# Performance work log

Hardware: AMD Instinct MI355X
Metric: run time of the kernel (lower is better)

The kernel has to match this reference:

```python
import jax, jax.numpy as jnp
import numpy as np

B, S, E, D = 8, 2048, 1024, 64


def setup_inputs() -> dict:
    key = jax.random.key(0)
    ks = jax.random.split(key, 8)
    x = jax.random.normal(ks[0], (B, S, E), dtype=jnp.float32)
    mask = jax.random.randint(ks[1], (B, S), 0, 2, dtype=jnp.int32)
    # torch.nn.Linear(E, D): weight [D, E], bias [D]; y = x @ W.T + b
    scale = 0.02
    Wq = jax.random.normal(ks[2], (D, E), dtype=jnp.float32) * scale
    bq = jax.random.normal(ks[3], (D,), dtype=jnp.float32) * scale
    Wk = jax.random.normal(ks[4], (D, E), dtype=jnp.float32) * scale
    bk = jax.random.normal(ks[5], (D,), dtype=jnp.float32) * scale
    Wv = jax.random.normal(ks[6], (D, E), dtype=jnp.float32) * scale
    bv = jax.random.normal(ks[7], (D,), dtype=jnp.float32) * scale
    return {"x": x, "mask": mask, "Wq": Wq, "bq": bq, "Wk": Wk, "bk": bk, "Wv": Wv, "bv": bv}


def reference(x, mask, Wq, bq, Wk, bk, Wv, bv):
    # Linear projections: [B,S,E] @ [E,D] -> [B,S,D]
    q = jnp.einsum('bse,de->bsd', x, Wq) + bq
    k = jnp.einsum('bse,de->bsd', x, Wk) + bk
    v = jnp.einsum('bse,de->bsd', x, Wv) + bv
    # scores: [B,S,S]
    scores = jnp.einsum('bid,bjd->bij', q, k) / np.sqrt(D).astype(np.float32)
    # Faithful mask replication: temp_mask[b,i,j] = mask[b,j] if j >= i else 0;
    # positions where temp_mask == 0 are filled with -1e22 (training=True).
    seq = scores.shape[1]
    upper = jnp.triu(jnp.ones((seq, seq), dtype=bool))        # j >= i
    valid = upper[None, :, :] & (mask[:, None, :] != 0)        # [B,S,S]
    scores = jnp.where(valid, scores, jnp.float32(-1e22))
    attn = jax.nn.softmax(scores, axis=-1)
    # out: [B,S,D]
    return jnp.einsum('bij,bjd->bid', attn, v)
```

## Files before the change

### kernel.cpp

```cpp
#include <hip/hip_runtime.h>
#include <hip/hip_bf16.h>

#define NB 8
#define NS 2048
#define NE 1024
#define ND 64

typedef __attribute__((ext_vector_type(8))) short bf16x8;
typedef __attribute__((ext_vector_type(4))) float f32x4;
typedef unsigned short u16;
typedef unsigned long long u64;

#define MFMA(a, b, c) __builtin_amdgcn_mfma_f32_16x16x32_bf16(a, b, c, 0, 0, 0)

__device__ __forceinline__ u16 f2bf(float f) {
  unsigned int u = __float_as_uint(f);
  u += 0x7fffu + ((u >> 16) & 1u);
  return (u16)(u >> 16);
}
__device__ __forceinline__ unsigned cvt2(float a, float b) {
  __hip_bfloat162 h = __float22bfloat162_rn(float2{a, b});
  return *(unsigned*)&h;
}

__device__ __forceinline__ void alds16(const void* g, void* l) {
  __builtin_amdgcn_global_load_lds(
      (const __attribute__((address_space(1))) unsigned int*)g,
      (__attribute__((address_space(3))) unsigned int*)l, 16, 0, 0);
}

__global__ void k0_prep(const float* __restrict__ Wq, const float* __restrict__ bq,
                        const float* __restrict__ Wk, const float* __restrict__ bk,
                        const float* __restrict__ Wv, const float* __restrict__ bv,
                        u16* __restrict__ Wcat2, float* __restrict__ bcat,
                        float* __restrict__ vmean) {
  int d = blockIdx.x * 256 + threadIdx.x;
  int c = d / 1536;
  int rem = d - c * 1536;
  int n = rem >> 3;
  int qp = rem & 7;
  int q = qp ^ (n & 7);
  const float* src = (n < 64) ? (Wq + n * NE) : (n < 128) ? (Wk + (n - 64) * NE)
                                                          : (Wv + (n - 128) * NE);
  const float* sp = src + c * 64 + q * 8;
  float4 a = *(const float4*)sp;
  float4 b = *(const float4*)(sp + 4);
  bf16x8 o;
  o[0] = (short)f2bf(a.x); o[1] = (short)f2bf(a.y);
  o[2] = (short)f2bf(a.z); o[3] = (short)f2bf(a.w);
  o[4] = (short)f2bf(b.x); o[5] = (short)f2bf(b.y);
  o[6] = (short)f2bf(b.z); o[7] = (short)f2bf(b.w);
  *(bf16x8*)&Wcat2[(size_t)d * 8] = o;
  if (blockIdx.x == 0) {
    int t = threadIdx.x;
    if (t < 192) bcat[t] = (t < 64) ? bq[t] : (t < 128) ? bk[t - 64] : bv[t - 128];
    vmean[t] = 0.f;
    vmean[t + 256] = 0.f;
  }
}

__global__ __launch_bounds__(256) void k1_qkv(
    const float* __restrict__ x, const u16* __restrict__ Wcat2,
    const float* __restrict__ bcat, u16* __restrict__ qb,
    u16* __restrict__ kbf2, u16* __restrict__ vtb2, float* __restrict__ vmean) {
  __shared__ float axs[2][32 * 64];
  __shared__ u16 bsb[2][192 * 64];
  const int t = threadIdx.x;
  const int m0 = blockIdx.x * 32;
  const int batch = m0 >> 11;
  const int sl = m0 & (NS - 1);
  const int w = t >> 6;
  const int l = t & 63;
  const int ln = l & 15;
  const int qd = l >> 4;
  const int n0 = w * 48;

  f32x4 zf = {0.f, 0.f, 0.f, 0.f};
  f32x4 acc[2][3] = {{zf, zf, zf}, {zf, zf, zf}};

  auto stageA = [&](int c, int buf) {
    #pragma unroll
    for (int i = 0; i < 2; ++i) {
      int rr = w * 8 + i * 4 + (l >> 4);
      int gch = (l & 15) ^ (rr & 7);
      const float* gp = x + (size_t)(m0 + rr) * NE + c * 64 + gch * 4;
      alds16(gp, &axs[buf][(w * 8 + i * 4) * 64]);
    }
  };
  auto stageB = [&](int c, int buf) {
    const u16* cb = Wcat2 + (size_t)c * 12288;
    #pragma unroll
    for (int i = 0; i < 6; ++i) {
      const u16* gp = cb + (w * 6 + i) * 512 + l * 8;
      alds16(gp, &bsb[buf][(w * 6 + i) * 512]);
    }
  };

  stageA(0, 0);
  stageB(0, 0);

  for (int c = 0; c < 16; ++c) {
    __syncthreads();
    if (c < 15) { stageA(c + 1, (c + 1) & 1); stageB(c + 1, (c + 1) & 1); }
    const int buf = c & 1;
    const int s = ln & 7;
    bf16x8 afr[2][2];
    #pragma unroll
    for (int mi = 0; mi < 2; ++mi) {
      int row = mi * 16 + ln;
      #pragma unroll
      for (int kc = 0; kc < 2; ++kc) {
        int g0 = kc * 8 + qd * 2;
        float4 fa = *(const float4*)&axs[buf][row * 64 + ((g0 ^ s) * 4)];
        float4 fb = *(const float4*)&axs[buf][row * 64 + (((g0 + 1) ^ s) * 4)];
        union { bf16x8 v; unsigned u[4]; } A;
        A.u[0] = cvt2(fa.x, fa.y); A.u[1] = cvt2(fa.z, fa.w);
        A.u[2] = cvt2(fb.x, fb.y); A.u[3] = cvt2(fb.z, fb.w);
        afr[mi][kc] = A.v;
      }
    }
    #pragma unroll
    for (int kc = 0; kc < 2; ++kc)
      #pragma unroll
      for (int nj = 0; nj < 3; ++nj) {
        int n = n0 + nj * 16 + ln;
        bf16x8 bb = *(const bf16x8*)&bsb[buf][n * 64 + (((kc * 4 + qd) ^ s) * 8)];
        acc[0][nj] = MFMA(afr[0][kc], bb, acc[0][nj]);
        acc[1][nj] = MFMA(afr[1][kc], bb, acc[1][nj]);
      }
  }

  #pragma unroll
  for (int nj = 0; nj < 3; ++nj) {
    int n = n0 + nj * 16 + ln;
    float bias = bcat[n];
    #pragma unroll
    for (int mi = 0; mi < 2; ++mi) {
      int jbase = sl + mi * 16 + qd * 4;
      if (n < 64) {
        #pragma unroll
        for (int r = 0; r < 4; ++r)
          qb[((size_t)batch * NS + jbase + r) * ND + n] = f2bf(acc[mi][nj][r] + bias);
      } else if (n < 128) {
        int d = n - 64;
        #pragma unroll
        for (int r = 0; r < 4; ++r) {
          int j = jbase + r;
          int pos = (((d >> 3) ^ (j & 7)) << 3) + (d & 7);
          kbf2[((size_t)batch * NS + j) * ND + pos] = f2bf(acc[mi][nj][r] + bias);
        }
      } else {
        int d = n - 128;
        int off = (jbase & ~63) + (((((jbase >> 5) & 1) ^ ((d >> 2) & 1))) << 5) +
                  (((((jbase >> 3) & 3) ^ (d & 3))) << 3) + (jbase & 7);
        ushort4 sv;
        sv.x = f2bf(acc[mi][nj][0] + bias); sv.y = f2bf(acc[mi][nj][1] + bias);
        sv.z = f2bf(acc[mi][nj][2] + bias); sv.w = f2bf(acc[mi][nj][3] + bias);
        *(ushort4*)&vtb2[((size_t)batch * ND + d) * NS + off] = sv;
      }
    }
    if (n >= 128) {
      float psum = acc[0][nj][0] + acc[0][nj][1] + acc[0][nj][2] + acc[0][nj][3] +
                   acc[1][nj][0] + acc[1][nj][1] + acc[1][nj][2] + acc[1][nj][3] +
                   8.f * bias;
      psum += __shfl_xor(psum, 16);
      psum += __shfl_xor(psum, 32);
      if (l < 16) atomicAdd(&vmean[batch * ND + (n - 128)], psum * (1.f / 2048.f));
    }
  }
}

__global__ __launch_bounds__(512, 4) void k3_attn(
    const u16* __restrict__ qb, const u16* __restrict__ kbf2,
    const u16* __restrict__ vtb2, const int* __restrict__ mask,
    const float* __restrict__ vmean, float* __restrict__ out) {
  __shared__ u16 ks[2][128 * 64];
  __shared__ u16 vs[2][64 * 128];
  __shared__ union {
    u16 ps[8][16 * 40];
    struct { float mb[2][16][68]; float mlb[2][16][16]; } m;
  } ub;

  const int g = blockIdx.x;
  const int tl = g >> 3;
  const int b = g & 7;
  const int i0 = tl * 32;
  const int j0f = i0 & ~127;
  const int np = (NS - j0f) >> 7;
  const int t = threadIdx.x;
  const int w = t >> 6;
  const int l = t & 63;
  const int ln = l & 15;
  const int qd = l >> 4;
  const int rg = w & 1;
  const int jg = w >> 1;

  const u16* qp = qb + ((size_t)b * NS + i0 + rg * 16 + ln) * ND + qd * 8;
  bf16x8 aq0 = *(const bf16x8*)qp;
  bf16x8 aq1 = *(const bf16x8*)(qp + 32);

  const u16* kB = kbf2 + (size_t)b * NS * ND;
  const u16* vB = vtb2 + (size_t)b * ND * NS;

  auto stage = [&](int it, int buf) {
    int j0 = j0f + it * 128;
    #pragma unroll
    for (int i = 0; i < 2; ++i) {
      int jl = w * 16 + i * 8;
      alds16(kB + (size_t)(j0 + jl) * ND + l * 8, &ks[buf][jl * 64]);
      int du = w * 2 + i;
      alds16(vB + (size_t)(du * 4 + (l >> 4)) * NS + j0 + (l & 15) * 8,
             &vs[buf][du * 512]);
    }
  };

  f32x4 zf = {0.f, 0.f, 0.f, 0.f};
  f32x4 od[4] = {zf, zf, zf, zf};
  float ls[4] = {0.f, 0.f, 0.f, 0.f};

  stage(0, 0);
  int mval = mask[b * NS + j0f + jg * 32 + (l & 31)];

  for (int it = 0; it < np; ++it) {
    u64 mv = __ballot(mval != 0);
    __syncthreads();
    if (it + 1 < np) {
      stage(it + 1, (it + 1) & 1);
      mval = mask[b * NS + j0f + (it + 1) * 128 + jg * 32 + (l & 31)];
    }
    const int buf = it & 1;
    const int jb = j0f + it * 128 + jg * 32;

    f32x4 sc[2] = {zf, zf};
    #pragma unroll
    for (int f = 0; f < 2; ++f) {
      const u16* kr = &ks[buf][(jg * 32 + f * 16 + ln) * 64];
      bf16x8 b0 = *(const bf16x8*)&kr[((qd ^ (ln & 7)) * 8)];
      bf16x8 b1 = *(const bf16x8*)&kr[(((4 + qd) ^ (ln & 7)) * 8)];
      sc[f] = MFMA(aq0, b0, sc[f]);
      sc[f] = MFMA(aq1, b1, sc[f]);
    }
    #pragma unroll
    for (int r = 0; r < 4; ++r) {
      const int i = i0 + rg * 16 + qd * 4 + r;
      #pragma unroll
      for (int f = 0; f < 2; ++f) {
        int jl = f * 16 + ln;
        bool ok = ((jb + jl) >= i) && (((mv >> jl) & 1ull) != 0);
        float p = ok ? __expf(sc[f][r] * 0.125f) : 0.f;
        ls[r] += p;
        ub.ps[w][(qd * 4 + r) * 40 + jl] = f2bf(p);
      }
    }
    bf16x8 pa = *(const bf16x8*)&ub.ps[w][ln * 40 + qd * 8];
    #pragma unroll
    for (int gx = 0; gx < 4; ++gx) {
      int unit = (jg >> 1) * 8 + (((jg & 1) ^ ((ln >> 2) & 1)) << 2) + (qd ^ (ln & 3));
      bf16x8 bv = *(const bf16x8*)&vs[buf][(gx * 16 + ln) * 128 + unit * 8];
      od[gx] = MFMA(pa, bv, od[gx]);
    }
  }

  __syncthreads();
  #pragma unroll 1
  for (int s = 3; s >= 1; --s) {
    if (jg == s) {
      #pragma unroll
      for (int r = 0; r < 4; ++r) {
        int row = qd * 4 + r;
        #pragma unroll
        for (int gx = 0; gx < 4; ++gx) ub.m.mb[rg][row][gx * 16 + ln] = od[gx][r];
        ub.m.mlb[rg][row][ln] = ls[r];
      }
    }
    __syncthreads();
    if (jg == s - 1) {
      #pragma unroll
      for (int r = 0; r < 4; ++r) {
        int row = qd * 4 + r;
        #pragma unroll
        for (int gx = 0; gx < 4; ++gx) od[gx][r] += ub.m.mb[rg][row][gx * 16 + ln];
        ls[r] += ub.m.mlb[rg][row][ln];
      }
    }
    __syncthreads();
  }

  if (jg == 0) {
    #pragma unroll
    for (int r = 0; r < 4; ++r) {
      #pragma unroll
      for (int o = 1; o < 16; o <<= 1) ls[r] += __shfl_xor(ls[r], o);
      int row = i0 + rg * 16 + qd * 4 + r;
      float* orow = out + ((size_t)b * NS + row) * ND;
      if (ls[r] > 0.f) {
        float inv = 1.f / ls[r];
        #pragma unroll
        for (int gx = 0; gx < 4; ++gx) orow[gx * 16 + ln] = od[gx][r] * inv;
      } else {
        #pragma unroll
        for (int gx = 0; gx < 4; ++gx) orow[gx * 16 + ln] = vmean[b * ND + gx * 16 + ln];
      }
    }
  }
}

extern "C" void kernel_launch(void* const* d_in, const int* in_sizes, int n_in,
                              void* d_out, int out_size, void* d_ws, size_t ws_size,
                              hipStream_t stream) {
  (void)in_sizes; (void)n_in; (void)out_size; (void)ws_size;
  const float* x = (const float*)d_in[0];
  const int* mask = (const int*)d_in[1];
  const float* Wq = (const float*)d_in[2];
  const float* bq = (const float*)d_in[3];
  const float* Wk = (const float*)d_in[4];
  const float* bk = (const float*)d_in[5];
  const float* Wv = (const float*)d_in[6];
  const float* bv = (const float*)d_in[7];
  float* out = (float*)d_out;

  char* ws = (char*)d_ws;
  u16* Wcat2 = (u16*)ws;
  float* bcat = (float*)(ws + 393216);
  float* vmean = (float*)(ws + 394240);
  u16* qb = (u16*)(ws + (1u << 20));
  u16* kbf2 = (u16*)(ws + (3u << 20));
  u16* vtb2 = (u16*)(ws + (5u << 20));

  hipLaunchKernelGGL(k0_prep, dim3(96), dim3(256), 0, stream,
                     Wq, bq, Wk, bk, Wv, bv, Wcat2, bcat, vmean);
  hipLaunchKernelGGL(k1_qkv, dim3(512), dim3(256), 0, stream,
                     x, Wcat2, bcat, qb, kbf2, vtb2, vmean);
  hipLaunchKernelGGL(k3_attn, dim3(512), dim3(512), 0, stream,
                     qb, kbf2, vtb2, mask, vmean, out);
}
```

Measured before the change: 144.7 us.

## Restructure QKV projection into 4-stage warp-specialized pipeline and rebalance attention tiles

```diff
diff --git a/kernel.cpp b/kernel.cpp
--- a/kernel.cpp
+++ b/kernel.cpp
@@ -12,6 +12,7 @@
 typedef unsigned long long u64;
 
 #define MFMA(a, b, c) __builtin_amdgcn_mfma_f32_16x16x32_bf16(a, b, c, 0, 0, 0)
+#define KEEPB(n) asm volatile("s_waitcnt vmcnt(" #n ")\n\ts_barrier" ::: "memory")
 
 __device__ __forceinline__ u16 f2bf(float f) {
   unsigned int u = __float_as_uint(f);
@@ -32,17 +33,16 @@
 __global__ void k0_prep(const float* __restrict__ Wq, const float* __restrict__ bq,
                         const float* __restrict__ Wk, const float* __restrict__ bk,
                         const float* __restrict__ Wv, const float* __restrict__ bv,
-                        u16* __restrict__ Wcat2, float* __restrict__ bcat,
+                        u16* __restrict__ Wcat3, float* __restrict__ bcat,
                         float* __restrict__ vmean) {
   int d = blockIdx.x * 256 + threadIdx.x;
-  int c = d / 1536;
-  int rem = d - c * 1536;
-  int n = rem >> 3;
-  int qp = rem & 7;
-  int q = qp ^ (n & 7);
+  int c = d / 768;
+  int rem = d - c * 768;
+  int n = rem >> 2;
+  int v = rem & 3;
   const float* src = (n < 64) ? (Wq + n * NE) : (n < 128) ? (Wk + (n - 64) * NE)
                                                           : (Wv + (n - 128) * NE);
-  const float* sp = src + c * 64 + q * 8;
+  const float* sp = src + c * 32 + v * 8;
   float4 a = *(const float4*)sp;
   float4 b = *(const float4*)(sp + 4);
   bf16x8 o;
@@ -50,7 +50,7 @@
   o[2] = (short)f2bf(a.z); o[3] = (short)f2bf(a.w);
   o[4] = (short)f2bf(b.x); o[5] = (short)f2bf(b.y);
   o[6] = (short)f2bf(b.z); o[7] = (short)f2bf(b.w);
-  *(bf16x8*)&Wcat2[(size_t)d * 8] = o;
+  *(bf16x8*)&Wcat3[(size_t)d * 8] = o;
   if (blockIdx.x == 0) {
     int t = threadIdx.x;
     if (t < 192) bcat[t] = (t < 64) ? bq[t] : (t < 128) ? bk[t - 64] : bv[t - 128];
@@ -59,12 +59,12 @@
   }
 }
 
-__global__ __launch_bounds__(256) void k1_qkv(
-    const float* __restrict__ x, const u16* __restrict__ Wcat2,
+__global__ __launch_bounds__(512) void k1_qkv(
+    const float* __restrict__ x, const u16* __restrict__ Wcat3,
     const float* __restrict__ bcat, u16* __restrict__ qb,
     u16* __restrict__ kbf2, u16* __restrict__ vtb2, float* __restrict__ vmean) {
-  __shared__ float axs[2][32 * 64];
-  __shared__ u16 bsb[2][192 * 64];
+  __shared__ float axs[4][1024];
+  __shared__ u16 bsb[4][6144];
   const int t = threadIdx.x;
   const int m0 = blockIdx.x * 32;
   const int batch = m0 >> 11;
@@ -73,104 +73,98 @@
   const int l = t & 63;
   const int ln = l & 15;
   const int qd = l >> 4;
-  const int n0 = w * 48;
+  const int rg = w & 1;
+  const int cg = w >> 1;
 
   f32x4 zf = {0.f, 0.f, 0.f, 0.f};
-  f32x4 acc[2][3] = {{zf, zf, zf}, {zf, zf, zf}};
-
-  auto stageA = [&](int c, int buf) {
-    #pragma unroll
-    for (int i = 0; i < 2; ++i) {
-      int rr = w * 8 + i * 4 + (l >> 4);
-      int gch = (l & 15) ^ (rr & 7);
-      const float* gp = x + (size_t)(m0 + rr) * NE + c * 64 + gch * 4;
-      alds16(gp, &axs[buf][(w * 8 + i * 4) * 64]);
+  f32x4 acc[3] = {zf, zf, zf};
+
+  auto stage = [&](int c, int buf) {
+    if (w < 2) {
+      #pragma unroll
+      for (int i = 0; i < 2; ++i) {
+        int un = w * 128 + i * 64 + l;
+        int row = un >> 3;
+        int q = (un & 7) ^ (row & 7);
+        alds16(x + (size_t)(m0 + row) * NE + c * 32 + q * 4,
+               &axs[buf][(w * 128 + i * 64) * 4]);
+      }
+    } else {
+      #pragma unroll
+      for (int i = 0; i < 2; ++i) {
+        int ub = (w - 2) * 128 + i * 64 + l;
+        int n = ub >> 2;
+        int v = (ub & 3) ^ ((n ^ (n >> 2)) & 3);
+        alds16(Wcat3 + (size_t)c * 6144 + n * 32 + v * 8,
+               &bsb[buf][((w - 2) * 128 + i * 64) * 8]);
+      }
     }
   };
-  auto stageB = [&](int c, int buf) {
-    const u16* cb = Wcat2 + (size_t)c * 12288;
-    #pragma unroll
-    for (int i = 0; i < 6; ++i) {
-      const u16* gp = cb + (w * 6 + i) * 512 + l * 8;
-      alds16(gp, &bsb[buf][(w * 6 + i) * 512]);
+
+  auto comp = [&](int buf) {
+    const int arow = rg * 16 + ln;
+    const int s = arow & 7;
+    float4 fa = *(const float4*)&axs[buf][arow * 32 + (((qd * 2) ^ s) << 2)];
+    float4 fb = *(const float4*)&axs[buf][arow * 32 + (((qd * 2 + 1) ^ s) << 2)];
+    union { bf16x8 v; unsigned u[4]; } A;
+    A.u[0] = cvt2(fa.x, fa.y); A.u[1] = cvt2(fa.z, fa.w);
+    A.u[2] = cvt2(fb.x, fb.y); A.u[3] = cvt2(fb.z, fb.w);
+    #pragma unroll
+    for (int nj = 0; nj < 3; ++nj) {
+      int n = cg * 48 + nj * 16 + ln;
+      int sw = (n ^ (n >> 2)) & 3;
+      bf16x8 bb = *(const bf16x8*)&bsb[buf][n * 32 + ((qd ^ sw) << 3)];
+      acc[nj] = MFMA(A.v, bb, acc[nj]);
     }
   };
 
-  stageA(0, 0);
-  stageB(0, 0);
-
-  for (int c = 0; c < 16; ++c) {
-    __syncthreads();
-    if (c < 15) { stageA(c + 1, (c + 1) & 1); stageB(c + 1, (c + 1) & 1); }
-    const int buf = c & 1;
-    const int s = ln & 7;
-    bf16x8 afr[2][2];
-    #pragma unroll
-    for (int mi = 0; mi < 2; ++mi) {
-      int row = mi * 16 + ln;
-      #pragma unroll
-      for (int kc = 0; kc < 2; ++kc) {
-        int g0 = kc * 8 + qd * 2;
-        float4 fa = *(const float4*)&axs[buf][row * 64 + ((g0 ^ s) * 4)];
-        float4 fb = *(const float4*)&axs[buf][row * 64 + (((g0 + 1) ^ s) * 4)];
-        union { bf16x8 v; unsigned u[4]; } A;
-        A.u[0] = cvt2(fa.x, fa.y); A.u[1] = cvt2(fa.z, fa.w);
-        A.u[2] = cvt2(fb.x, fb.y); A.u[3] = cvt2(fb.z, fb.w);
-        afr[mi][kc] = A.v;
-      }
-    }
-    #pragma unroll
-    for (int kc = 0; kc < 2; ++kc)
-      #pragma unroll
-      for (int nj = 0; nj < 3; ++nj) {
-        int n = n0 + nj * 16 + ln;
-        bf16x8 bb = *(const bf16x8*)&bsb[buf][n * 64 + (((kc * 4 + qd) ^ s) * 8)];
-        acc[0][nj] = MFMA(afr[0][kc], bb, acc[0][nj]);
-        acc[1][nj] = MFMA(afr[1][kc], bb, acc[1][nj]);
-      }
-  }
-
+  stage(0, 0);
+  stage(1, 1);
+  stage(2, 2);
+  for (int c = 0; c < 29; ++c) {
+    KEEPB(4);
+    stage(c + 3, (c + 3) & 3);
+    comp(c & 3);
+  }
+  KEEPB(4); comp(1);
+  KEEPB(2); comp(2);
+  KEEPB(0); comp(3);
+
+  const float QS = 0.125f;
   #pragma unroll
   for (int nj = 0; nj < 3; ++nj) {
-    int n = n0 + nj * 16 + ln;
+    int n = cg * 48 + nj * 16 + ln;
     float bias = bcat[n];
-    #pragma unroll
-    for (int mi = 0; mi < 2; ++mi) {
-      int jbase = sl + mi * 16 + qd * 4;
-      if (n < 64) {
-        #pragma unroll
-        for (int r = 0; r < 4; ++r)
-          qb[((size_t)batch * NS + jbase + r) * ND + n] = f2bf(acc[mi][nj][r] + bias);
-      } else if (n < 128) {
-        int d = n - 64;
-        #pragma unroll
-        for (int r = 0; r < 4; ++r) {
-          int j = jbase + r;
-          int pos = (((d >> 3) ^ (j & 7)) << 3) + (d & 7);
-          kbf2[((size_t)batch * NS + j) * ND + pos] = f2bf(acc[mi][nj][r] + bias);
-        }
-      } else {
-        int d = n - 128;
-        int off = (jbase & ~63) + (((((jbase >> 5) & 1) ^ ((d >> 2) & 1))) << 5) +
-                  (((((jbase >> 3) & 3) ^ (d & 3))) << 3) + (jbase & 7);
-        ushort4 sv;
-        sv.x = f2bf(acc[mi][nj][0] + bias); sv.y = f2bf(acc[mi][nj][1] + bias);
-        sv.z = f2bf(acc[mi][nj][2] + bias); sv.w = f2bf(acc[mi][nj][3] + bias);
-        *(ushort4*)&vtb2[((size_t)batch * ND + d) * NS + off] = sv;
-      }
-    }
-    if (n >= 128) {
-      float psum = acc[0][nj][0] + acc[0][nj][1] + acc[0][nj][2] + acc[0][nj][3] +
-                   acc[1][nj][0] + acc[1][nj][1] + acc[1][nj][2] + acc[1][nj][3] +
-                   8.f * bias;
+    int jbase = sl + rg * 16 + qd * 4;
+    if (n < 64) {
+      #pragma unroll
+      for (int r = 0; r < 4; ++r)
+        qb[((size_t)batch * NS + jbase + r) * ND + n] = f2bf((acc[nj][r] + bias) * QS);
+    } else if (n < 128) {
+      int d = n - 64;
+      #pragma unroll
+      for (int r = 0; r < 4; ++r) {
+        int j = jbase + r;
+        int pos = (((d >> 3) ^ (j & 7)) << 3) + (d & 7);
+        kbf2[((size_t)batch * NS + j) * ND + pos] = f2bf(acc[nj][r] + bias);
+      }
+    } else {
+      int d = n - 128;
+      int off = (jbase & ~63) + (((((jbase >> 5) & 1) ^ ((d >> 2) & 1))) << 5) +
+                (((((jbase >> 3) & 3) ^ (d & 3))) << 3) + (jbase & 7);
+      ushort4 sv;
+      sv.x = f2bf(acc[nj][0] + bias); sv.y = f2bf(acc[nj][1] + bias);
+      sv.z = f2bf(acc[nj][2] + bias); sv.w = f2bf(acc[nj][3] + bias);
+      *(ushort4*)&vtb2[((size_t)batch * ND + d) * NS + off] = sv;
+      float psum = acc[nj][0] + acc[nj][1] + acc[nj][2] + acc[nj][3] + 4.f * bias;
       psum += __shfl_xor(psum, 16);
       psum += __shfl_xor(psum, 32);
-      if (l < 16) atomicAdd(&vmean[batch * ND + (n - 128)], psum * (1.f / 2048.f));
-    }
-  }
-}
-
-__global__ __launch_bounds__(512, 4) void k3_attn(
+      if (l < 16) atomicAdd(&vmean[batch * ND + d], psum * (1.f / 2048.f));
+    }
+  }
+}
+
+__global__ __launch_bounds__(512) void k3_attn(
     const u16* __restrict__ qb, const u16* __restrict__ kbf2,
     const u16* __restrict__ vtb2, const int* __restrict__ mask,
     const float* __restrict__ vmean, float* __restrict__ out) {
@@ -182,9 +176,10 @@
   } ub;
 
   const int g = blockIdx.x;
-  const int tl = g >> 3;
   const int b = g & 7;
-  const int i0 = tl * 32;
+  const int uu = g >> 3;
+  const int tile = (uu & 1) ? (63 - (uu >> 1)) : (uu >> 1);
+  const int i0 = tile * 32;
   const int j0f = i0 & ~127;
   const int np = (NS - j0f) >> 7;
   const int t = threadIdx.x;
@@ -217,11 +212,12 @@
   f32x4 zf = {0.f, 0.f, 0.f, 0.f};
   f32x4 od[4] = {zf, zf, zf, zf};
   float ls[4] = {0.f, 0.f, 0.f, 0.f};
+  const int pvunit = (jg >> 1) * 8 + (((jg & 1) ^ ((ln >> 2) & 1)) << 2) + (qd ^ (ln & 3));
 
   stage(0, 0);
   int mval = mask[b * NS + j0f + jg * 32 + (l & 31)];
 
-  for (int it = 0; it < np; ++it) {
+  auto body = [&](int it, bool causal) {
     u64 mv = __ballot(mval != 0);
     __syncthreads();
     if (it + 1 < np) {
@@ -246,8 +242,8 @@
       #pragma unroll
       for (int f = 0; f < 2; ++f) {
         int jl = f * 16 + ln;
-        bool ok = ((jb + jl) >= i) && (((mv >> jl) & 1ull) != 0);
-        float p = ok ? __expf(sc[f][r] * 0.125f) : 0.f;
+        bool ok = (((mv >> jl) & 1ull) != 0) && (!causal || (jb + jl >= i));
+        float p = ok ? __expf(sc[f][r]) : 0.f;
         ls[r] += p;
         ub.ps[w][(qd * 4 + r) * 40 + jl] = f2bf(p);
       }
@@ -255,11 +251,13 @@
     bf16x8 pa = *(const bf16x8*)&ub.ps[w][ln * 40 + qd * 8];
     #pragma unroll
     for (int gx = 0; gx < 4; ++gx) {
-      int unit = (jg >> 1) * 8 + (((jg & 1) ^ ((ln >> 2) & 1)) << 2) + (qd ^ (ln & 3));
-      bf16x8 bv = *(const bf16x8*)&vs[buf][(gx * 16 + ln) * 128 + unit * 8];
+      bf16x8 bv = *(const bf16x8*)&vs[buf][(gx * 16 + ln) * 128 + pvunit * 8];
       od[gx] = MFMA(pa, bv, od[gx]);
     }
-  }
+  };
+
+  body(0, true);
+  for (int it = 1; it < np; ++it) body(it, false);
 
   __syncthreads();
   #pragma unroll 1
@@ -320,7 +318,7 @@
   float* out = (float*)d_out;
 
   char* ws = (char*)d_ws;
-  u16* Wcat2 = (u16*)ws;
+  u16* Wcat3 = (u16*)ws;
   float* bcat = (float*)(ws + 393216);
   float* vmean = (float*)(ws + 394240);
   u16* qb = (u16*)(ws + (1u << 20));
@@ -328,9 +326,9 @@
   u16* vtb2 = (u16*)(ws + (5u << 20));
 
   hipLaunchKernelGGL(k0_prep, dim3(96), dim3(256), 0, stream,
-                     Wq, bq, Wk, bk, Wv, bv, Wcat2, bcat, vmean);
-  hipLaunchKernelGGL(k1_qkv, dim3(512), dim3(256), 0, stream,
-                     x, Wcat2, bcat, qb, kbf2, vtb2, vmean);
+                     Wq, bq, Wk, bk, Wv, bv, Wcat3, bcat, vmean);
+  hipLaunchKernelGGL(k1_qkv, dim3(512), dim3(512), 0, stream,
+                     x, Wcat3, bcat, qb, kbf2, vtb2, vmean);
   hipLaunchKernelGGL(k3_attn, dim3(512), dim3(512), 0, stream,
                      qb, kbf2, vtb2, mask, vmean, out);
 }
```

Result: no change. 146.5 us (+1.3%).
